# Kernel tuning notes

Measured on AMD Instinct MI355X. Metric: run time of the kernel, lower is better.

The kernel has to match this reference:

```python
import jax, jax.numpy as jnp
import numpy as np

N, E, D, A = 50000, 1_600_000, 32, 2
H1, C1, H2, C2 = 4, 16, 2, 32  # GATv2Conv(D,16,heads=4) -> 64; GATv2Conv(64,32,heads=2) -> 64


def setup_inputs() -> dict:
    key = jax.random.key(0)
    ks = jax.random.split(key, 16)

    def glorot(k, shape):
        fan = shape[0] + shape[-1]
        return jax.random.normal(k, shape, jnp.float32) * np.float32(np.sqrt(2.0 / fan))

    return {
        "x": jax.random.normal(ks[0], (N, D), jnp.float32),
        "edge_index": jax.random.randint(ks[1], (2, E), 0, N),
        "edge_attr": jax.random.normal(ks[2], (E, 2), jnp.float32),
        # GATv2 layer 1 (lin_l/lin_r with bias, lin_edge no bias, att [H,C], out bias)
        "w1_l": glorot(ks[3], (D, H1 * C1)), "b1_l": jnp.zeros((H1 * C1,), jnp.float32),
        "w1_r": glorot(ks[4], (D, H1 * C1)), "b1_r": jnp.zeros((H1 * C1,), jnp.float32),
        "w1_e": glorot(ks[5], (2, H1 * C1)),
        "att1": glorot(ks[6], (H1, C1)),
        "bias1": jnp.zeros((H1 * C1,), jnp.float32),
        # GATv2 layer 2
        "w2_l": glorot(ks[7], (H1 * C1, H2 * C2)), "b2_l": jnp.zeros((H2 * C2,), jnp.float32),
        "w2_r": glorot(ks[8], (H1 * C1, H2 * C2)), "b2_r": jnp.zeros((H2 * C2,), jnp.float32),
        "w2_e": glorot(ks[9], (2, H2 * C2)),
        "att2": glorot(ks[10], (H2, C2)),
        "bias2": jnp.zeros((H2 * C2,), jnp.float32),
        # heads
        "w_actor": glorot(ks[11], (H2 * C2, A)), "b_actor": jnp.zeros((A,), jnp.float32),
        "w_critic": glorot(ks[12], (H2 * C2, 1)), "b_critic": jnp.zeros((1,), jnp.float32),
        "log_std": jnp.zeros((A,), jnp.float32),
    }


def _gatv2(x, src, dst, eattr, Wl, bl, Wr, br, We, att, bias, H, C, n):
    # PyG GATv2Conv: message j->i with i = dst, j = src
    xl = (x @ Wl + bl).reshape(n, H, C)  # source-side transform (x_j)
    xr = (x @ Wr + br).reshape(n, H, C)  # target-side transform (x_i)
    ee = (eattr @ We).reshape(-1, H, C)  # per-edge embedding
    z = jax.nn.leaky_relu(xl[src] + xr[dst] + ee, 0.2)  # [Etot, H, C]
    logits = jnp.einsum('ehc,hc->eh', z, att)  # [Etot, H]
    # segment softmax over incoming edges of each dst node
    m = jax.ops.segment_max(logits, dst, num_segments=n)
    p = jnp.exp(logits - m[dst])
    denom = jax.ops.segment_sum(p, dst, num_segments=n)
    alpha = p / denom[dst]  # every node has a self-loop -> denom > 0
    msg = xl[src] * alpha[:, :, None]  # [Etot, H, C]
    out = jax.ops.segment_sum(msg, dst, num_segments=n)
    return out.reshape(n, H * C) + bias


def reference(x, edge_index, edge_attr,
              w1_l, b1_l, w1_r, b1_r, w1_e, att1, bias1,
              w2_l, b2_l, w2_r, b2_r, w2_e, att2, bias2,
              w_actor, b_actor, w_critic, b_critic, log_std):
    src, dst = edge_index[0], edge_index[1]
    # add_self_loops=True, fill_value='mean': self-loop edge_attr = mean of incoming edge_attr
    cnt = jax.ops.segment_sum(jnp.ones((edge_attr.shape[0],), x.dtype), dst, num_segments=N)
    sums = jax.ops.segment_sum(edge_attr, dst, num_segments=N)
    loop_attr = sums / jnp.maximum(cnt, 1.0)[:, None]
    loop = jnp.arange(N, dtype=src.dtype)
    src_f = jnp.concatenate([src, loop])
    dst_f = jnp.concatenate([dst, loop])
    ea = jnp.concatenate([edge_attr, loop_attr], axis=0)

    h = jax.nn.relu(_gatv2(x, src_f, dst_f, ea, w1_l, b1_l, w1_r, b1_r, w1_e, att1, bias1, H1, C1, N))
    h = jax.nn.relu(_gatv2(h, src_f, dst_f, ea, w2_l, b2_l, w2_r, b2_r, w2_e, att2, bias2, H2, C2, N))

    action_mean = jnp.tanh(h @ w_actor + b_actor)  # [N, A]
    value = h @ w_critic + b_critic               # [N, 1]
    std = jnp.exp(log_std)                        # [A]  (Normal(action_mean, std))
    return action_mean, std, value
```

## Files before the change

kernel.cpp:

```cpp
#include <hip/hip_runtime.h>
#include <hip/hip_fp16.h>
#include <math.h>

#define DIN   32
#define F1    64
#define F2    64

typedef __attribute__((ext_vector_type(2))) float f32x2;

__device__ __forceinline__ f32x2 pkfma(f32x2 a, f32x2 b, f32x2 c) {
#if __has_builtin(__builtin_elementwise_fma)
    return __builtin_elementwise_fma(a, b, c);
#else
    return a * b + c;
#endif
}
__device__ __forceinline__ f32x2 pkmax(f32x2 a, f32x2 b) {
    f32x2 r; r.x = fmaxf(a.x, b.x); r.y = fmaxf(a.y, b.y); return r;
}

__device__ __forceinline__ unsigned bf16pack(float a, float b) {
    unsigned ua = __float_as_uint(a);
    unsigned ub = __float_as_uint(b);
    ua = (ua + 0x7FFFu + ((ua >> 16) & 1u)) >> 16;
    ub = (ub + 0x7FFFu + ((ub >> 16) & 1u)) >> 16;
    return ua | (ub << 16);
}

template <int K>
__device__ __forceinline__ void lin_lr_body(int bid,
        const float* __restrict__ x,
        const float* __restrict__ Wl, const float* __restrict__ bl,
        const float* __restrict__ Wr, const float* __restrict__ br,
        __half* __restrict__ xl, float* __restrict__ xr, int n) {
    __shared__ float Ash[32][K + 4];
    __shared__ float Wsh[K][128];
    const int t = threadIdx.x;
    const int node0 = bid * 32;

    for (int idx = t; idx < 32 * (K / 4); idx += 256) {
        int m = idx / (K / 4), kq = idx % (K / 4);
        float4 v = make_float4(0.f, 0.f, 0.f, 0.f);
        if (node0 + m < n) v = ((const float4*)(x + (size_t)(node0 + m) * K))[kq];
        *(float4*)&Ash[m][kq * 4] = v;
    }
    for (int idx = t; idx < K * 32; idx += 256) {
        int k = idx / 32, j4 = idx % 32;
        float4 v = (j4 < 16) ? ((const float4*)(Wl + (size_t)k * 64))[j4]
                             : ((const float4*)(Wr + (size_t)k * 64))[j4 - 16];
        *(float4*)&Wsh[k][j4 * 4] = v;
    }
    __syncthreads();

    const int ty = t >> 4;
    const int tx = t & 15;
    f32x2 c0[4], c1[4];
#pragma unroll
    for (int j = 0; j < 4; j++) {
        c0[j].x = 0.f; c0[j].y = 0.f;
        c1[j].x = 0.f; c1[j].y = 0.f;
    }

#pragma unroll 4
    for (int k = 0; k < K; k++) {
        float a0 = Ash[ty * 2 + 0][k];
        float a1 = Ash[ty * 2 + 1][k];
        float4 w0 = *(const float4*)&Wsh[k][tx * 8];
        float4 w1 = *(const float4*)&Wsh[k][tx * 8 + 4];
        f32x2 wv0; wv0.x = w0.x; wv0.y = w0.y;
        f32x2 wv1; wv1.x = w0.z; wv1.y = w0.w;
        f32x2 wv2; wv2.x = w1.x; wv2.y = w1.y;
        f32x2 wv3; wv3.x = w1.z; wv3.y = w1.w;
        f32x2 a0s; a0s.x = a0; a0s.y = a0;
        f32x2 a1s; a1s.x = a1; a1s.y = a1;
        c0[0] = pkfma(a0s, wv0, c0[0]);
        c0[1] = pkfma(a0s, wv1, c0[1]);
        c0[2] = pkfma(a0s, wv2, c0[2]);
        c0[3] = pkfma(a0s, wv3, c0[3]);
        c1[0] = pkfma(a1s, wv0, c1[0]);
        c1[1] = pkfma(a1s, wv1, c1[1]);
        c1[2] = pkfma(a1s, wv2, c1[2]);
        c1[3] = pkfma(a1s, wv3, c1[3]);
    }

    const float* bsrc = (tx < 8) ? bl : br;
    int jb = (tx < 8) ? tx * 8 : (tx - 8) * 8;
    float4 b0 = ((const float4*)(bsrc + jb))[0];
    float4 b1 = ((const float4*)(bsrc + jb))[1];
#pragma unroll
    for (int m = 0; m < 2; m++) {
        int node = node0 + ty * 2 + m;
        if (node >= n) continue;
        const f32x2* cc = (m == 0) ? c0 : c1;
        float o0 = cc[0].x + b0.x, o1 = cc[0].y + b0.y;
        float o2 = cc[1].x + b0.z, o3 = cc[1].y + b0.w;
        float o4 = cc[2].x + b1.x, o5 = cc[2].y + b1.y;
        float o6 = cc[3].x + b1.z, o7 = cc[3].y + b1.w;
        if (tx < 8) {
            __half2 h0 = __floats2half2_rn(o0, o1);
            __half2 h1 = __floats2half2_rn(o2, o3);
            __half2 h2 = __floats2half2_rn(o4, o5);
            __half2 h3 = __floats2half2_rn(o6, o7);
            uint4 pk;
            pk.x = *(unsigned*)&h0; pk.y = *(unsigned*)&h1;
            pk.z = *(unsigned*)&h2; pk.w = *(unsigned*)&h3;
            *((uint4*)(xl + (size_t)node * 64 + jb)) = pk;
        } else {
            float4 f0 = make_float4(o0, o1, o2, o3);
            float4 f1 = make_float4(o4, o5, o6, o7);
            ((float4*)(xr + (size_t)node * 64 + jb))[0] = f0;
            ((float4*)(xr + (size_t)node * 64 + jb))[1] = f1;
        }
    }
}

__global__ __launch_bounds__(256, 2)
void fused_bcount_lin1(const int* __restrict__ dstr, int* __restrict__ cursor,
                       int* __restrict__ chunkoff, int* __restrict__ rank,
                       int E, int Ec, int NB, int gridLin,
                       const float* __restrict__ x,
                       const float* __restrict__ Wl, const float* __restrict__ bl,
                       const float* __restrict__ Wr, const float* __restrict__ br,
                       __half* __restrict__ xl, float* __restrict__ xr, int n) {
    __shared__ int hist[256];
    if ((int)blockIdx.x < gridLin) {
        lin_lr_body<DIN>(blockIdx.x, x, Wl, bl, Wr, br, xl, xr, n);
        return;
    }
    const int blk = blockIdx.x - gridLin;
    const int t = threadIdx.x;
    hist[t] = 0;
    __syncthreads();
    const int s0 = blk * Ec, s1 = min(E, s0 + Ec);
    for (int e = s0 + t; e < s1; e += 256)
        rank[e] = atomicAdd(&hist[dstr[e] >> 8], 1);
    __syncthreads();
    if (t < NB) {
        int h = hist[t];
        chunkoff[blk * 256 + t] = h ? atomicAdd(&cursor[t], h) : 0;
    }
}

__global__ __launch_bounds__(512)
void scatter_buckets(const int* __restrict__ srcr, const int* __restrict__ dstr,
                     const float* __restrict__ ea, const int* __restrict__ rank,
                     const int* __restrict__ chunkoff,
                     int2* __restrict__ inter, int E, int Ec, int NB, int cap) {
    __shared__ int colsh[256];
    const int blk = blockIdx.x;
    const int t = threadIdx.x;
    if (t < 256) colsh[t] = (t < NB) ? (t * cap + chunkoff[blk * 256 + t]) : 0;
    __syncthreads();
    const int s0 = blk * Ec, s1 = min(E, s0 + Ec);
    for (int e = s0 + t; e < s1; e += 512) {
        int d = dstr[e];
        float2 v = ((const float2*)ea)[e];
        int2 r;
        r.x = srcr[e] | ((d & 255) << 24);
        r.y = (int)bf16pack(v.x, v.y);
        inter[colsh[d >> 8] + rank[e]] = r;
    }
}

__global__ __launch_bounds__(512)
void bucket_csr(const int2* __restrict__ inter, const int* __restrict__ cursor,
                int2* __restrict__ rse, float2* __restrict__ la2,
                int2* __restrict__ edges, int NB, int N, int cap) {
    __shared__ int sh[256];
    __shared__ int cur[256];
    const int b = blockIdx.x, t = threadIdx.x;
    const int bstart = b * cap;
    const int bend = bstart + cursor[b];

    if (t < 256) sh[t] = 0;
    __syncthreads();
    for (int pos = bstart + t; pos < bend; pos += 512)
        atomicAdd(&sh[((unsigned)inter[pos].x) >> 24], 1);
    __syncthreads();
    int cnt_v = 0, myrs = 0;
    if (t < 256) cnt_v = sh[t];
    __syncthreads();
    if (t < 256) sh[t] = cnt_v;
    __syncthreads();
    for (int off = 1; off < 256; off <<= 1) {
        int x = (t >= off && t < 256) ? sh[t - off] : 0;
        __syncthreads();
        if (t < 256) sh[t] += x;
        __syncthreads();
    }
    if (t < 256) {
        int excl = sh[t] - cnt_v;
        cur[t] = excl;
        myrs = bstart + excl;
        int node = b * 256 + t;
        if (node < N) rse[node] = make_int2(myrs, myrs + cnt_v);
    }
    __syncthreads();
    for (int pos = bstart + t; pos < bend; pos += 512) {
        int2 r = inter[pos];
        int k = atomicAdd(&cur[((unsigned)r.x) >> 24], 1);
        r.x &= 0x00FFFFFF;
        edges[bstart + k] = r;
    }
    int zend = (b + 1) * cap + ((b == NB - 1) ? 64 : 0);
    for (int pos = bend + t; pos < zend; pos += 512)
        edges[pos] = make_int2(0, 0);
    __syncthreads();
    if (t < 256) {
        int node = b * 256 + t;
        if (node < N) {
            float s0 = 0.f, s1 = 0.f;
            for (int pos = myrs; pos < myrs + cnt_v; pos++) {
                int2 rec = edges[pos];
                s0 += __int_as_float(rec.y << 16);
                s1 += __int_as_float(rec.y & 0xFFFF0000);
            }
            float inv = cnt_v ? 1.0f / (float)cnt_v : 0.f;
            la2[node] = make_float2(s0 * inv, s1 * inv);
        }
    }
}

__global__ __launch_bounds__(256, 2)
void lin_lr_tiled64(const float* __restrict__ x,
                    const float* __restrict__ Wl, const float* __restrict__ bl,
                    const float* __restrict__ Wr, const float* __restrict__ br,
                    __half* __restrict__ xl, float* __restrict__ xr, int n) {
    lin_lr_body<F1>(blockIdx.x, x, Wl, bl, Wr, br, xl, xr, n);
}

template <int H, int C, bool FUSE_HEADS>
__global__ __launch_bounds__(256)
void gat_kernel(const __half* __restrict__ xl, const float* __restrict__ xr,
                const int2* __restrict__ rse, const float2* __restrict__ la2,
                const int2* __restrict__ edges,
                const float* __restrict__ We, const float* __restrict__ att,
                const float* __restrict__ bias, float* __restrict__ hout,
                const float* __restrict__ wa, const float* __restrict__ ba,
                const float* __restrict__ wc, const float* __restrict__ bc,
                const float* __restrict__ ls, float* __restrict__ pout,
                int n) {
    constexpr int LPH = C / 4;
    if (FUSE_HEADS && blockIdx.x == 0 && threadIdx.x < 2)
        pout[(size_t)n * 2 + threadIdx.x] = expf(ls[threadIdx.x]);
    const int lane = threadIdx.x & 63;
    const int wid = (blockIdx.x * blockDim.x + threadIdx.x) >> 6;
    if (wid >= n) return;
    const int i = wid;
    const int g = lane >> 4;
    const int q = lane & 15;

    const uint2* xlh = (const uint2*)xl;
    const float4 xri4 = ((const float4*)(xr + (size_t)i * 64))[q];
    const float4 we04 = ((const float4*)We)[q];
    const float4 we14 = ((const float4*)(We + 64))[q];
    const float4 av4 = ((const float4*)att)[q];
    const float LOG2E = 1.4426950408889634f;
    f32x2 xrlo; xrlo.x = xri4.x; xrlo.y = xri4.y;
    f32x2 xrhi; xrhi.x = xri4.z; xrhi.y = xri4.w;
    f32x2 we0lo; we0lo.x = we04.x; we0lo.y = we04.y;
    f32x2 we0hi; we0hi.x = we04.z; we0hi.y = we04.w;
    f32x2 we1lo; we1lo.x = we14.x; we1lo.y = we14.y;
    f32x2 we1hi; we1hi.x = we14.z; we1hi.y = we14.w;
    f32x2 avlo; avlo.x = av4.x * LOG2E; avlo.y = av4.y * LOG2E;
    f32x2 avhi; avhi.x = av4.z * LOG2E; avhi.y = av4.w * LOG2E;

    auto h4lo = [](uint2 h) -> f32x2 {
        float2 a = __half22float2(*(__half2*)&h.x);
        f32x2 r; r.x = a.x; r.y = a.y; return r;
    };
    auto h4hi = [](uint2 h) -> f32x2 {
        float2 b = __half22float2(*(__half2*)&h.y);
        f32x2 r; r.x = b.x; r.y = b.y; return r;
    };
    auto logit_of = [&](f32x2 xlo, f32x2 xhi, float ea0, float ea1) -> float {
        f32x2 e0; e0.x = ea0; e0.y = ea0;
        f32x2 e1; e1.x = ea1; e1.y = ea1;
        f32x2 ylo = xlo + pkfma(e0, we0lo, pkfma(e1, we1lo, xrlo));
        f32x2 yhi = xhi + pkfma(e0, we0hi, pkfma(e1, we1hi, xrhi));
        ylo = pkmax(ylo, ylo * 0.2f);
        yhi = pkmax(yhi, yhi * 0.2f);
        f32x2 l2 = pkfma(ylo, avlo, yhi * avhi);
        return l2.x + l2.y;
    };

    float den = 0.f;
    f32x2 aclo; aclo.x = 0.f; aclo.y = 0.f;
    f32x2 achi; achi.x = 0.f; achi.y = 0.f;

    const int2 se = rse[i];
    const int e0 = se.x, e1 = se.y;
    const int r = (e1 - e0) & 7;

    if (r) {
        int2 h0 = edges[e0 + g];
        int2 h1 = edges[e0 + 4 + g];
        uint2 u0 = xlh[(h0.x << 4) + q];
        uint2 u1 = xlh[(h1.x << 4) + q];
        f32x2 x0lo = h4lo(u0), x0hi = h4hi(u0);
        f32x2 x1lo = h4lo(u1), x1hi = h4hi(u1);
        const bool v0 = g < r;
        const bool v1 = (4 + g) < r;
        float ea00 = v0 ? __int_as_float(h0.y << 16) : 0.f;
        float ea01 = v0 ? __int_as_float(h0.y & 0xFFFF0000) : 0.f;
        float ea10 = v1 ? __int_as_float(h1.y << 16) : 0.f;
        float ea11 = v1 ? __int_as_float(h1.y & 0xFFFF0000) : 0.f;
        float l0 = logit_of(x0lo, x0hi, ea00, ea01);
        float l1 = logit_of(x1lo, x1hi, ea10, ea11);
#pragma unroll
        for (int m = 1; m < LPH; m <<= 1) {
            l0 += __shfl_xor(l0, m, 64);
            l1 += __shfl_xor(l1, m, 64);
        }
        float p0 = v0 ? exp2f(l0) : 0.f;
        float p1 = v1 ? exp2f(l1) : 0.f;
        den += p0 + p1;
        f32x2 p0s; p0s.x = p0; p0s.y = p0;
        f32x2 p1s; p1s.x = p1; p1s.y = p1;
        aclo = pkfma(p0s, x0lo, pkfma(p1s, x1lo, aclo));
        achi = pkfma(p0s, x0hi, pkfma(p1s, x1hi, achi));
    }

    const int em = e0 + r;
    int2 rn0 = edges[em + g];
    int2 rn1 = edges[em + 4 + g];
    uint2 xpn0 = xlh[(rn0.x << 4) + q];
    uint2 xpn1 = xlh[(rn1.x << 4) + q];

    for (int eb = em; eb < e1; eb += 8) {
        int2 r0 = rn0, r1 = rn1;
        f32x2 x0lo = h4lo(xpn0), x0hi = h4hi(xpn0);
        f32x2 x1lo = h4lo(xpn1), x1hi = h4hi(xpn1);
        rn0 = edges[eb + 8 + g];
        rn1 = edges[eb + 12 + g];
        xpn0 = xlh[(rn0.x << 4) + q];
        xpn1 = xlh[(rn1.x << 4) + q];

        float ea00 = __int_as_float(r0.y << 16);
        float ea01 = __int_as_float(r0.y & 0xFFFF0000);
        float ea10 = __int_as_float(r1.y << 16);
        float ea11 = __int_as_float(r1.y & 0xFFFF0000);

        float l0 = logit_of(x0lo, x0hi, ea00, ea01);
        float l1 = logit_of(x1lo, x1hi, ea10, ea11);
#pragma unroll
        for (int m = 1; m < LPH; m <<= 1) {
            l0 += __shfl_xor(l0, m, 64);
            l1 += __shfl_xor(l1, m, 64);
        }
        float p0 = exp2f(l0);
        float p1 = exp2f(l1);
        den += p0 + p1;
        f32x2 p0s; p0s.x = p0; p0s.y = p0;
        f32x2 p1s; p1s.x = p1; p1s.y = p1;
        aclo = pkfma(p0s, x0lo, pkfma(p1s, x1lo, aclo));
        achi = pkfma(p0s, x0hi, pkfma(p1s, x1hi, achi));
    }

    float a0 = aclo.x, a1 = aclo.y, a2 = achi.x, a3 = achi.y;

#pragma unroll
    for (int m = 16; m < 64; m <<= 1) {
        den += __shfl_xor(den, m, 64);
        a0 += __shfl_xor(a0, m, 64);
        a1 += __shfl_xor(a1, m, 64);
        a2 += __shfl_xor(a2, m, 64);
        a3 += __shfl_xor(a3, m, 64);
    }

    const float2 lam = la2[i];
    uint2 us = xlh[(i << 4) + q];
    f32x2 xslo = h4lo(us), xshi = h4hi(us);
    {
        float l = logit_of(xslo, xshi, lam.x, lam.y);
#pragma unroll
        for (int m = 1; m < LPH; m <<= 1) l += __shfl_xor(l, m, 64);
        float p = exp2f(l);
        den += p;
        a0 = fmaf(p, xslo.x, a0);
        a1 = fmaf(p, xslo.y, a1);
        a2 = fmaf(p, xshi.x, a2);
        a3 = fmaf(p, xshi.y, a3);
    }

    float rd = 1.0f / den;
    const float4 bv = ((const float4*)bias)[q];
    float4 o;
    o.x = fmaxf(fmaf(a0, rd, bv.x), 0.f);
    o.y = fmaxf(fmaf(a1, rd, bv.y), 0.f);
    o.z = fmaxf(fmaf(a2, rd, bv.z), 0.f);
    o.w = fmaxf(fmaf(a3, rd, bv.w), 0.f);

    if (!FUSE_HEADS) {
        if (g == 0) ((float4*)(hout + (size_t)i * 64))[q] = o;
    } else {
        float4 wa01 = ((const float4*)wa)[q * 2];
        float4 wa23 = ((const float4*)wa)[q * 2 + 1];
        float4 wcv  = ((const float4*)wc)[q];
        float d0 = o.x * wa01.x + o.y * wa01.z + o.z * wa23.x + o.w * wa23.z;
        float d1 = o.x * wa01.y + o.y * wa01.w + o.z * wa23.y + o.w * wa23.w;
        float d2 = o.x * wcv.x + o.y * wcv.y + o.z * wcv.z + o.w * wcv.w;
#pragma unroll
        for (int m = 1; m < 16; m <<= 1) {
            d0 += __shfl_xor(d0, m, 64);
            d1 += __shfl_xor(d1, m, 64);
            d2 += __shfl_xor(d2, m, 64);
        }
        if (lane == 0) {
            pout[(size_t)i * 2 + 0] = tanhf(d0 + ba[0]);
            pout[(size_t)i * 2 + 1] = tanhf(d1 + ba[1]);
            pout[(size_t)n * 2 + 2 + i] = d2 + bc[0];
        }
    }
}


extern "C" void kernel_launch(void* const* d_in, const int* in_sizes, int n_in,
                              void* d_out, int out_size, void* d_ws, size_t ws_size,
                              hipStream_t stream) {
    const float* x    = (const float*)d_in[0];
    const int*   ei   = (const int*)  d_in[1];
    const float* ea   = (const float*)d_in[2];
    const float* w1l  = (const float*)d_in[3];
    const float* b1l  = (const float*)d_in[4];
    const float* w1r  = (const float*)d_in[5];
    const float* b1r  = (const float*)d_in[6];
    const float* w1e  = (const float*)d_in[7];
    const float* att1 = (const float*)d_in[8];
    const float* bias1= (const float*)d_in[9];
    const float* w2l  = (const float*)d_in[10];
    const float* b2l  = (const float*)d_in[11];
    const float* w2r  = (const float*)d_in[12];
    const float* b2r  = (const float*)d_in[13];
    const float* w2e  = (const float*)d_in[14];
    const float* att2 = (const float*)d_in[15];
    const float* bias2= (const float*)d_in[16];
    const float* wa   = (const float*)d_in[17];
    const float* ba   = (const float*)d_in[18];
    const float* wc   = (const float*)d_in[19];
    const float* bc   = (const float*)d_in[20];
    const float* ls   = (const float*)d_in[21];

    const int N = in_sizes[0] / DIN;
    const int E = in_sizes[2] / 2;
    const int* srcr = ei;
    const int* dstr = ei + E;

    const int NB = (N + 255) >> 8;
    const int Ec = (E + 255) / 256;
    int cap = (E + NB - 1) / NB;
    cap = ((cap + cap / 4) + 63) & ~63;

    char* p = (char*)d_ws;
    auto alloc = [&](size_t bytes) -> void* {
        void* r = (void*)p;
        p += (bytes + 255) & ~(size_t)255;
        return r;
    };
    int*    cursor   = (int*)   alloc(256 * 4);
    int*    chunkoff = (int*)   alloc(256 * 256 * 4);
    int*    rank     = (int*)   alloc((size_t)E * 4);
    int2*   rse      = (int2*)  alloc((size_t)N * 8);
    float2* la2      = (float2*)alloc((size_t)N * 8);
    int2*   edges    = (int2*)  alloc(((size_t)NB * cap + 64) * 8);
    __half* xl       = (__half*)alloc((size_t)N * F1 * 2);
    float*  xr       = (float*) alloc((size_t)N * F1 * 4);
    float*  h1       = (float*) alloc((size_t)N * F1 * 4);
    float*  h2       = (float*) alloc((size_t)N * F2 * 4);
    int2* inter = (int2*)h1;
    (void)ws_size; (void)n_in; (void)out_size;

    hipMemsetAsync(cursor, 0, 256 * 4, stream);

    const int TB = 256;
    int gridGemm = (N + 31) / 32;
    int gridWave = (N + 3) / 4;

    fused_bcount_lin1<<<gridGemm + 256, TB, 0, stream>>>(
        dstr, cursor, chunkoff, rank, E, Ec, NB, gridGemm,
        x, w1l, b1l, w1r, b1r, xl, xr, N);
    scatter_buckets<<<256, 512, 0, stream>>>(srcr, dstr, ea, rank, chunkoff,
                                             inter, E, Ec, NB, cap);
    bucket_csr<<<NB, 512, 0, stream>>>(inter, cursor, rse, la2, edges, NB, N, cap);

    gat_kernel<4, 16, false><<<gridWave, TB, 0, stream>>>(
        xl, xr, rse, la2, edges, w1e, att1, bias1, h1,
        nullptr, nullptr, nullptr, nullptr, nullptr, nullptr, N);
    lin_lr_tiled64<<<gridGemm, TB, 0, stream>>>(h1, w2l, b2l, w2r, b2r, xl, xr, N);
    gat_kernel<2, 32, true><<<gridWave, TB, 0, stream>>>(
        xl, xr, rse, la2, edges, w2e, att2, bias2, h2,
        wa, ba, wc, bc, ls, (float*)d_out, N);
}
```

Before: 297.6 us.

## Split GAT aggregation into two feature-half passes with separate head kernel

Each GAT layer now runs as two launches, each covering 32 of the 64 features. Every wave processes 16 edges per iteration with 8 lanes per edge instead of 4 lanes over 8 edges. The gathered source-feature working set per pass is halved, which is meant to improve cache hit rates on the random xl gathers. In exchange, the edge list is read twice and the per-edge logit work is redone. The actor/critic heads move out of the second GAT kernel into their own kernel that reads h2, adding a launch and an extra pass over h2.

```diff
diff --git a/kernel.cpp b/kernel.cpp
--- a/kernel.cpp
+++ b/kernel.cpp
@@ -229,32 +229,27 @@
     lin_lr_body<F1>(blockIdx.x, x, Wl, bl, Wr, br, xl, xr, n);
 }
 
-template <int H, int C, bool FUSE_HEADS>
+template <int LPH>
 __global__ __launch_bounds__(256)
-void gat_kernel(const __half* __restrict__ xl, const float* __restrict__ xr,
-                const int2* __restrict__ rse, const float2* __restrict__ la2,
-                const int2* __restrict__ edges,
-                const float* __restrict__ We, const float* __restrict__ att,
-                const float* __restrict__ bias, float* __restrict__ hout,
-                const float* __restrict__ wa, const float* __restrict__ ba,
-                const float* __restrict__ wc, const float* __restrict__ bc,
-                const float* __restrict__ ls, float* __restrict__ pout,
-                int n) {
-    constexpr int LPH = C / 4;
-    if (FUSE_HEADS && blockIdx.x == 0 && threadIdx.x < 2)
-        pout[(size_t)n * 2 + threadIdx.x] = expf(ls[threadIdx.x]);
+void gat_slice(const __half* __restrict__ xl, const float* __restrict__ xr,
+               const int2* __restrict__ rse, const float2* __restrict__ la2,
+               const int2* __restrict__ edges,
+               const float* __restrict__ We, const float* __restrict__ att,
+               const float* __restrict__ bias, float* __restrict__ hout,
+               int n, int slice) {
     const int lane = threadIdx.x & 63;
     const int wid = (blockIdx.x * blockDim.x + threadIdx.x) >> 6;
     if (wid >= n) return;
     const int i = wid;
-    const int g = lane >> 4;
-    const int q = lane & 15;
+    const int g = lane >> 3;
+    const int q = lane & 7;
+    const int so2 = slice * 8;
 
     const uint2* xlh = (const uint2*)xl;
-    const float4 xri4 = ((const float4*)(xr + (size_t)i * 64))[q];
-    const float4 we04 = ((const float4*)We)[q];
-    const float4 we14 = ((const float4*)(We + 64))[q];
-    const float4 av4 = ((const float4*)att)[q];
+    const float4 xri4 = ((const float4*)(xr + (size_t)i * 64 + slice * 32))[q];
+    const float4 we04 = ((const float4*)(We + slice * 32))[q];
+    const float4 we14 = ((const float4*)(We + 64 + slice * 32))[q];
+    const float4 av4  = ((const float4*)(att + slice * 32))[q];
     const float LOG2E = 1.4426950408889634f;
     f32x2 xrlo; xrlo.x = xri4.x; xrlo.y = xri4.y;
     f32x2 xrhi; xrhi.x = xri4.z; xrhi.y = xri4.w;
@@ -290,17 +285,17 @@
 
     const int2 se = rse[i];
     const int e0 = se.x, e1 = se.y;
-    const int r = (e1 - e0) & 7;
+    const int r = (e1 - e0) & 15;
 
     if (r) {
         int2 h0 = edges[e0 + g];
-        int2 h1 = edges[e0 + 4 + g];
-        uint2 u0 = xlh[(h0.x << 4) + q];
-        uint2 u1 = xlh[(h1.x << 4) + q];
+        int2 h1 = edges[e0 + 8 + g];
+        uint2 u0 = xlh[(h0.x << 4) + so2 + q];
+        uint2 u1 = xlh[(h1.x << 4) + so2 + q];
         f32x2 x0lo = h4lo(u0), x0hi = h4hi(u0);
         f32x2 x1lo = h4lo(u1), x1hi = h4hi(u1);
         const bool v0 = g < r;
-        const bool v1 = (4 + g) < r;
+        const bool v1 = (8 + g) < r;
         float ea00 = v0 ? __int_as_float(h0.y << 16) : 0.f;
         float ea01 = v0 ? __int_as_float(h0.y & 0xFFFF0000) : 0.f;
         float ea10 = v1 ? __int_as_float(h1.y << 16) : 0.f;
@@ -323,18 +318,18 @@
 
     const int em = e0 + r;
     int2 rn0 = edges[em + g];
-    int2 rn1 = edges[em + 4 + g];
-    uint2 xpn0 = xlh[(rn0.x << 4) + q];
-    uint2 xpn1 = xlh[(rn1.x << 4) + q];
-
-    for (int eb = em; eb < e1; eb += 8) {
+    int2 rn1 = edges[em + 8 + g];
+    uint2 xpn0 = xlh[(rn0.x << 4) + so2 + q];
+    uint2 xpn1 = xlh[(rn1.x << 4) + so2 + q];
+
+    for (int eb = em; eb < e1; eb += 16) {
         int2 r0 = rn0, r1 = rn1;
         f32x2 x0lo = h4lo(xpn0), x0hi = h4hi(xpn0);
         f32x2 x1lo = h4lo(xpn1), x1hi = h4hi(xpn1);
-        rn0 = edges[eb + 8 + g];
-        rn1 = edges[eb + 12 + g];
-        xpn0 = xlh[(rn0.x << 4) + q];
-        xpn1 = xlh[(rn1.x << 4) + q];
+        rn0 = edges[eb + 16 + g];
+        rn1 = edges[eb + 24 + g];
+        xpn0 = xlh[(rn0.x << 4) + so2 + q];
+        xpn1 = xlh[(rn1.x << 4) + so2 + q];
 
         float ea00 = __int_as_float(r0.y << 16);
         float ea01 = __int_as_float(r0.y & 0xFFFF0000);
@@ -360,7 +355,7 @@
     float a0 = aclo.x, a1 = aclo.y, a2 = achi.x, a3 = achi.y;
 
 #pragma unroll
-    for (int m = 16; m < 64; m <<= 1) {
+    for (int m = 8; m < 64; m <<= 1) {
         den += __shfl_xor(den, m, 64);
         a0 += __shfl_xor(a0, m, 64);
         a1 += __shfl_xor(a1, m, 64);
@@ -369,7 +364,7 @@
     }
 
     const float2 lam = la2[i];
-    uint2 us = xlh[(i << 4) + q];
+    uint2 us = xlh[(i << 4) + so2 + q];
     f32x2 xslo = h4lo(us), xshi = h4hi(us);
     {
         float l = logit_of(xslo, xshi, lam.x, lam.y);
@@ -384,33 +379,49 @@
     }
 
     float rd = 1.0f / den;
-    const float4 bv = ((const float4*)bias)[q];
+    const float4 bv = ((const float4*)(bias + slice * 32))[q];
     float4 o;
     o.x = fmaxf(fmaf(a0, rd, bv.x), 0.f);
     o.y = fmaxf(fmaf(a1, rd, bv.y), 0.f);
     o.z = fmaxf(fmaf(a2, rd, bv.z), 0.f);
     o.w = fmaxf(fmaf(a3, rd, bv.w), 0.f);
 
-    if (!FUSE_HEADS) {
-        if (g == 0) ((float4*)(hout + (size_t)i * 64))[q] = o;
-    } else {
-        float4 wa01 = ((const float4*)wa)[q * 2];
-        float4 wa23 = ((const float4*)wa)[q * 2 + 1];
-        float4 wcv  = ((const float4*)wc)[q];
-        float d0 = o.x * wa01.x + o.y * wa01.z + o.z * wa23.x + o.w * wa23.z;
-        float d1 = o.x * wa01.y + o.y * wa01.w + o.z * wa23.y + o.w * wa23.w;
-        float d2 = o.x * wcv.x + o.y * wcv.y + o.z * wcv.z + o.w * wcv.w;
-#pragma unroll
-        for (int m = 1; m < 16; m <<= 1) {
-            d0 += __shfl_xor(d0, m, 64);
-            d1 += __shfl_xor(d1, m, 64);
-            d2 += __shfl_xor(d2, m, 64);
-        }
-        if (lane == 0) {
-            pout[(size_t)i * 2 + 0] = tanhf(d0 + ba[0]);
-            pout[(size_t)i * 2 + 1] = tanhf(d1 + ba[1]);
-            pout[(size_t)n * 2 + 2 + i] = d2 + bc[0];
-        }
+    if (g == 0)
+        ((float4*)(hout + (size_t)i * 64 + slice * 32))[q] = o;
+}
+
+__global__ __launch_bounds__(256)
+void actor_critic_head(const float* __restrict__ h2,
+                       const float* __restrict__ wa, const float* __restrict__ ba,
+                       const float* __restrict__ wc, const float* __restrict__ bc,
+                       const float* __restrict__ ls, float* __restrict__ pout,
+                       int n) {
+    if (blockIdx.x == 0 && threadIdx.x < 2)
+        pout[(size_t)n * 2 + threadIdx.x] = expf(ls[threadIdx.x]);
+    const int lane = threadIdx.x & 63;
+    const int sub = lane >> 4;
+    const int q = lane & 15;
+    const int wid = (blockIdx.x * blockDim.x + threadIdx.x) >> 6;
+    const int i = wid * 4 + sub;
+    if (i >= n) return;
+
+    float4 o = ((const float4*)(h2 + (size_t)i * 64))[q];
+    float4 wa01 = ((const float4*)wa)[q * 2];
+    float4 wa23 = ((const float4*)wa)[q * 2 + 1];
+    float4 wcv  = ((const float4*)wc)[q];
+    float d0 = o.x * wa01.x + o.y * wa01.z + o.z * wa23.x + o.w * wa23.z;
+    float d1 = o.x * wa01.y + o.y * wa01.w + o.z * wa23.y + o.w * wa23.w;
+    float d2 = o.x * wcv.x + o.y * wcv.y + o.z * wcv.z + o.w * wcv.w;
+#pragma unroll
+    for (int m = 1; m < 16; m <<= 1) {
+        d0 += __shfl_xor(d0, m, 64);
+        d1 += __shfl_xor(d1, m, 64);
+        d2 += __shfl_xor(d2, m, 64);
+    }
+    if (q == 0) {
+        pout[(size_t)i * 2 + 0] = tanhf(d0 + ba[0]);
+        pout[(size_t)i * 2 + 1] = tanhf(d1 + ba[1]);
+        pout[(size_t)n * 2 + 2 + i] = d2 + bc[0];
     }
 }
 
@@ -475,6 +486,7 @@
     const int TB = 256;
     int gridGemm = (N + 31) / 32;
     int gridWave = (N + 3) / 4;
+    int gridHead = (N + 15) / 16;
 
     fused_bcount_lin1<<<gridGemm + 256, TB, 0, stream>>>(
         dstr, cursor, chunkoff, rank, E, Ec, NB, gridGemm,
@@ -483,11 +495,18 @@
                                              inter, E, Ec, NB, cap);
     bucket_csr<<<NB, 512, 0, stream>>>(inter, cursor, rse, la2, edges, NB, N, cap);
 
-    gat_kernel<4, 16, false><<<gridWave, TB, 0, stream>>>(
-        xl, xr, rse, la2, edges, w1e, att1, bias1, h1,
-        nullptr, nullptr, nullptr, nullptr, nullptr, nullptr, N);
+    gat_slice<4><<<gridWave, TB, 0, stream>>>(
+        xl, xr, rse, la2, edges, w1e, att1, bias1, h1, N, 0);
+    gat_slice<4><<<gridWave, TB, 0, stream>>>(
+        xl, xr, rse, la2, edges, w1e, att1, bias1, h1, N, 1);
+
     lin_lr_tiled64<<<gridGemm, TB, 0, stream>>>(h1, w2l, b2l, w2r, b2r, xl, xr, N);
-    gat_kernel<2, 32, true><<<gridWave, TB, 0, stream>>>(
-        xl, xr, rse, la2, edges, w2e, att2, bias2, h2,
-        wa, ba, wc, bc, ls, (float*)d_out, N);
-}
+
+    gat_slice<8><<<gridWave, TB, 0, stream>>>(
+        xl, xr, rse, la2, edges, w2e, att2, bias2, h2, N, 0);
+    gat_slice<8><<<gridWave, TB, 0, stream>>>(
+        xl, xr, rse, la2, edges, w2e, att2, bias2, h2, N, 1);
+
+    actor_critic_head<<<gridHead, TB, 0, stream>>>(
+        h2, wa, ba, wc, bc, ls, (float*)d_out, N);
+}
```

Result: slower. 347.8 us (+16.9%).

## Replace two-level bucket CSR build with global per-node atomic count, scan, scatter

Applied to the files above, without the earlier changes.

The two-level bucketed CSR construction (per-chunk bucket histogram, scatter into padded buckets, per-bucket local sort) is replaced by per-node global atomic counting, a block-level prefix scan that recomputes the running prefix sum in each block, and a direct scatter into the final edge array. The self-loop mean edge attribute is no longer precomputed per node. Instead the GAT kernel accumulates edge-attribute sums while it walks the incoming edges and divides by the degree, which removes the separate la2 array. The intent is to drop one full pass over the edges and the padded intermediate buffer. The cost is global atomics contended on 50k counters, a scan whose per-block prefix loop re-reads up to N counters, and extra shuffle reductions in both GAT passes.

```diff
diff --git a/kernel.cpp b/kernel.cpp
--- a/kernel.cpp
+++ b/kernel.cpp
@@ -115,109 +115,71 @@
 }
 
 __global__ __launch_bounds__(256, 2)
-void fused_bcount_lin1(const int* __restrict__ dstr, int* __restrict__ cursor,
-                       int* __restrict__ chunkoff, int* __restrict__ rank,
-                       int E, int Ec, int NB, int gridLin,
-                       const float* __restrict__ x,
-                       const float* __restrict__ Wl, const float* __restrict__ bl,
-                       const float* __restrict__ Wr, const float* __restrict__ br,
-                       __half* __restrict__ xl, float* __restrict__ xr, int n) {
-    __shared__ int hist[256];
+void fused_count_lin1(const int* __restrict__ dstr, int* __restrict__ cnt,
+                      int* __restrict__ rank, int E, int Ec, int gridLin,
+                      const float* __restrict__ x,
+                      const float* __restrict__ Wl, const float* __restrict__ bl,
+                      const float* __restrict__ Wr, const float* __restrict__ br,
+                      __half* __restrict__ xl, float* __restrict__ xr, int n) {
     if ((int)blockIdx.x < gridLin) {
         lin_lr_body<DIN>(blockIdx.x, x, Wl, bl, Wr, br, xl, xr, n);
         return;
     }
     const int blk = blockIdx.x - gridLin;
     const int t = threadIdx.x;
-    hist[t] = 0;
-    __syncthreads();
     const int s0 = blk * Ec, s1 = min(E, s0 + Ec);
     for (int e = s0 + t; e < s1; e += 256)
-        rank[e] = atomicAdd(&hist[dstr[e] >> 8], 1);
+        rank[e] = atomicAdd(&cnt[dstr[e]], 1);
+}
+
+__global__ __launch_bounds__(256)
+void scan_rse(const int* __restrict__ cnt, int2* __restrict__ rse,
+              int2* __restrict__ edges, int N, int E) {
+    __shared__ int sh[256];
+    const int b = blockIdx.x, t = threadIdx.x;
+    if (b == 0 && t < 64) edges[E + t] = make_int2(0, 0);
+    const int base = b * 256;
+    int pre = 0;
+    for (int idx = t; idx < base; idx += 256) pre += cnt[idx];
+    sh[t] = pre;
+    for (int off = 128; off > 0; off >>= 1) {
+        __syncthreads();
+        if (t < off) sh[t] += sh[t + off];
+    }
     __syncthreads();
-    if (t < NB) {
-        int h = hist[t];
-        chunkoff[blk * 256 + t] = h ? atomicAdd(&cursor[t], h) : 0;
+    const int off0 = sh[0];
+    __syncthreads();
+    const int node = base + t;
+    const int c = (node < N) ? cnt[node] : 0;
+    sh[t] = c;
+    __syncthreads();
+    for (int off = 1; off < 256; off <<= 1) {
+        int x = (t >= off) ? sh[t - off] : 0;
+        __syncthreads();
+        sh[t] += x;
+        __syncthreads();
+    }
+    if (node < N) {
+        int excl = sh[t] - c;
+        rse[node] = make_int2(off0 + excl, off0 + excl + c);
     }
 }
 
 __global__ __launch_bounds__(512)
-void scatter_buckets(const int* __restrict__ srcr, const int* __restrict__ dstr,
-                     const float* __restrict__ ea, const int* __restrict__ rank,
-                     const int* __restrict__ chunkoff,
-                     int2* __restrict__ inter, int E, int Ec, int NB, int cap) {
-    __shared__ int colsh[256];
+void scatter_edges(const int* __restrict__ srcr, const int* __restrict__ dstr,
+                   const float* __restrict__ ea, const int* __restrict__ rank,
+                   const int2* __restrict__ rse, int2* __restrict__ edges,
+                   int E, int Ec) {
     const int blk = blockIdx.x;
     const int t = threadIdx.x;
-    if (t < 256) colsh[t] = (t < NB) ? (t * cap + chunkoff[blk * 256 + t]) : 0;
-    __syncthreads();
     const int s0 = blk * Ec, s1 = min(E, s0 + Ec);
     for (int e = s0 + t; e < s1; e += 512) {
         int d = dstr[e];
         float2 v = ((const float2*)ea)[e];
         int2 r;
-        r.x = srcr[e] | ((d & 255) << 24);
+        r.x = srcr[e];
         r.y = (int)bf16pack(v.x, v.y);
-        inter[colsh[d >> 8] + rank[e]] = r;
-    }
-}
-
-__global__ __launch_bounds__(512)
-void bucket_csr(const int2* __restrict__ inter, const int* __restrict__ cursor,
-                int2* __restrict__ rse, float2* __restrict__ la2,
-                int2* __restrict__ edges, int NB, int N, int cap) {
-    __shared__ int sh[256];
-    __shared__ int cur[256];
-    const int b = blockIdx.x, t = threadIdx.x;
-    const int bstart = b * cap;
-    const int bend = bstart + cursor[b];
-
-    if (t < 256) sh[t] = 0;
-    __syncthreads();
-    for (int pos = bstart + t; pos < bend; pos += 512)
-        atomicAdd(&sh[((unsigned)inter[pos].x) >> 24], 1);
-    __syncthreads();
-    int cnt_v = 0, myrs = 0;
-    if (t < 256) cnt_v = sh[t];
-    __syncthreads();
-    if (t < 256) sh[t] = cnt_v;
-    __syncthreads();
-    for (int off = 1; off < 256; off <<= 1) {
-        int x = (t >= off && t < 256) ? sh[t - off] : 0;
-        __syncthreads();
-        if (t < 256) sh[t] += x;
-        __syncthreads();
-    }
-    if (t < 256) {
-        int excl = sh[t] - cnt_v;
-        cur[t] = excl;
-        myrs = bstart + excl;
-        int node = b * 256 + t;
-        if (node < N) rse[node] = make_int2(myrs, myrs + cnt_v);
-    }
-    __syncthreads();
-    for (int pos = bstart + t; pos < bend; pos += 512) {
-        int2 r = inter[pos];
-        int k = atomicAdd(&cur[((unsigned)r.x) >> 24], 1);
-        r.x &= 0x00FFFFFF;
-        edges[bstart + k] = r;
-    }
-    int zend = (b + 1) * cap + ((b == NB - 1) ? 64 : 0);
-    for (int pos = bend + t; pos < zend; pos += 512)
-        edges[pos] = make_int2(0, 0);
-    __syncthreads();
-    if (t < 256) {
-        int node = b * 256 + t;
-        if (node < N) {
-            float s0 = 0.f, s1 = 0.f;
-            for (int pos = myrs; pos < myrs + cnt_v; pos++) {
-                int2 rec = edges[pos];
-                s0 += __int_as_float(rec.y << 16);
-                s1 += __int_as_float(rec.y & 0xFFFF0000);
-            }
-            float inv = cnt_v ? 1.0f / (float)cnt_v : 0.f;
-            la2[node] = make_float2(s0 * inv, s1 * inv);
-        }
+        edges[rse[d].x + rank[e]] = r;
     }
 }
 
@@ -232,7 +194,7 @@
 template <int H, int C, bool FUSE_HEADS>
 __global__ __launch_bounds__(256)
 void gat_kernel(const __half* __restrict__ xl, const float* __restrict__ xr,
-                const int2* __restrict__ rse, const float2* __restrict__ la2,
+                const int2* __restrict__ rse,
                 const int2* __restrict__ edges,
                 const float* __restrict__ We, const float* __restrict__ att,
                 const float* __restrict__ bias, float* __restrict__ hout,
@@ -285,6 +247,7 @@
     };
 
     float den = 0.f;
+    float sea0 = 0.f, sea1 = 0.f;
     f32x2 aclo; aclo.x = 0.f; aclo.y = 0.f;
     f32x2 achi; achi.x = 0.f; achi.y = 0.f;
 
@@ -305,6 +268,8 @@
         float ea01 = v0 ? __int_as_float(h0.y & 0xFFFF0000) : 0.f;
         float ea10 = v1 ? __int_as_float(h1.y << 16) : 0.f;
         float ea11 = v1 ? __int_as_float(h1.y & 0xFFFF0000) : 0.f;
+        sea0 += ea00 + ea10;
+        sea1 += ea01 + ea11;
         float l0 = logit_of(x0lo, x0hi, ea00, ea01);
         float l1 = logit_of(x1lo, x1hi, ea10, ea11);
 #pragma unroll
@@ -340,6 +305,8 @@
         float ea01 = __int_as_float(r0.y & 0xFFFF0000);
         float ea10 = __int_as_float(r1.y << 16);
         float ea11 = __int_as_float(r1.y & 0xFFFF0000);
+        sea0 += ea00 + ea10;
+        sea1 += ea01 + ea11;
 
         float l0 = logit_of(x0lo, x0hi, ea00, ea01);
         float l1 = logit_of(x1lo, x1hi, ea10, ea11);
@@ -366,13 +333,18 @@
         a1 += __shfl_xor(a1, m, 64);
         a2 += __shfl_xor(a2, m, 64);
         a3 += __shfl_xor(a3, m, 64);
-    }
-
-    const float2 lam = la2[i];
+        sea0 += __shfl_xor(sea0, m, 64);
+        sea1 += __shfl_xor(sea1, m, 64);
+    }
+
+    const int cnt_i = e1 - e0;
+    const float invc = cnt_i ? 1.0f / (float)cnt_i : 0.f;
+    const float lamx = sea0 * invc;
+    const float lamy = sea1 * invc;
     uint2 us = xlh[(i << 4) + q];
     f32x2 xslo = h4lo(us), xshi = h4hi(us);
     {
-        float l = logit_of(xslo, xshi, lam.x, lam.y);
+        float l = logit_of(xslo, xshi, lamx, lamy);
 #pragma unroll
         for (int m = 1; m < LPH; m <<= 1) l += __shfl_xor(l, m, 64);
         float p = exp2f(l);
@@ -448,8 +420,6 @@
 
     const int NB = (N + 255) >> 8;
     const int Ec = (E + 255) / 256;
-    int cap = (E + NB - 1) / NB;
-    cap = ((cap + cap / 4) + 63) & ~63;
 
     char* p = (char*)d_ws;
     auto alloc = [&](size_t bytes) -> void* {
@@ -457,37 +427,34 @@
         p += (bytes + 255) & ~(size_t)255;
         return r;
     };
-    int*    cursor   = (int*)   alloc(256 * 4);
-    int*    chunkoff = (int*)   alloc(256 * 256 * 4);
-    int*    rank     = (int*)   alloc((size_t)E * 4);
-    int2*   rse      = (int2*)  alloc((size_t)N * 8);
-    float2* la2      = (float2*)alloc((size_t)N * 8);
-    int2*   edges    = (int2*)  alloc(((size_t)NB * cap + 64) * 8);
-    __half* xl       = (__half*)alloc((size_t)N * F1 * 2);
-    float*  xr       = (float*) alloc((size_t)N * F1 * 4);
-    float*  h1       = (float*) alloc((size_t)N * F1 * 4);
-    float*  h2       = (float*) alloc((size_t)N * F2 * 4);
-    int2* inter = (int2*)h1;
+    int*    cnt   = (int*)   alloc((size_t)NB * 256 * 4);
+    int*    rank  = (int*)   alloc((size_t)E * 4);
+    int2*   rse   = (int2*)  alloc((size_t)N * 8);
+    int2*   edges = (int2*)  alloc(((size_t)E + 64) * 8);
+    __half* xl    = (__half*)alloc((size_t)N * F1 * 2);
+    float*  xr    = (float*) alloc((size_t)N * F1 * 4);
+    float*  h1    = (float*) alloc((size_t)N * F1 * 4);
+    float*  h2    = (float*) alloc((size_t)N * F2 * 4);
     (void)ws_size; (void)n_in; (void)out_size;
 
-    hipMemsetAsync(cursor, 0, 256 * 4, stream);
+    hipMemsetAsync(cnt, 0, (size_t)NB * 256 * 4, stream);
 
     const int TB = 256;
     int gridGemm = (N + 31) / 32;
     int gridWave = (N + 3) / 4;
 
-    fused_bcount_lin1<<<gridGemm + 256, TB, 0, stream>>>(
-        dstr, cursor, chunkoff, rank, E, Ec, NB, gridGemm,
+    fused_count_lin1<<<gridGemm + 256, TB, 0, stream>>>(
+        dstr, cnt, rank, E, Ec, gridGemm,
         x, w1l, b1l, w1r, b1r, xl, xr, N);
-    scatter_buckets<<<256, 512, 0, stream>>>(srcr, dstr, ea, rank, chunkoff,
-                                             inter, E, Ec, NB, cap);
-    bucket_csr<<<NB, 512, 0, stream>>>(inter, cursor, rse, la2, edges, NB, N, cap);
+    scan_rse<<<NB, 256, 0, stream>>>(cnt, rse, edges, N, E);
+    scatter_edges<<<256, 512, 0, stream>>>(srcr, dstr, ea, rank, rse,
+                                           edges, E, Ec);
 
     gat_kernel<4, 16, false><<<gridWave, TB, 0, stream>>>(
-        xl, xr, rse, la2, edges, w1e, att1, bias1, h1,
+        xl, xr, rse, edges, w1e, att1, bias1, h1,
         nullptr, nullptr, nullptr, nullptr, nullptr, nullptr, N);
     lin_lr_tiled64<<<gridGemm, TB, 0, stream>>>(h1, w2l, b2l, w2r, b2r, xl, xr, N);
     gat_kernel<2, 32, true><<<gridWave, TB, 0, stream>>>(
-        xl, xr, rse, la2, edges, w2e, att2, bias2, h2,
+        xl, xr, rse, edges, w2e, att2, bias2, h2,
         wa, ba, wc, bc, ls, (float*)d_out, N);
 }
```

Result: slower. 360.9 us (+21.3%).

## Fuse bucket count with scatter and compute self-loop edge mean inside GAT kernel

Applied to the files above, without the earlier changes.

The bucket histogram and scatter phases are merged into one kernel. Per-edge ranks are kept in shared memory as 16-bit values instead of going through global rank/chunkoff arrays, and the number of chunks rises to 512 so each chunk fits the shared buffer. The serial per-node self-loop mean loop in bucket_csr is removed. The GAT kernels instead accumulate edge-attribute sums while walking each node's edges and reduce them across the wavefront, which saves a launch and global round trips in exchange for a few extra shuffles per node. Both GAT layers recompute the mean, and the 3584-entry shared buffer assumes the edge count per chunk stays within that bound.

```diff
diff --git a/kernel.cpp b/kernel.cpp
--- a/kernel.cpp
+++ b/kernel.cpp
@@ -115,57 +115,49 @@
 }
 
 __global__ __launch_bounds__(256, 2)
-void fused_bcount_lin1(const int* __restrict__ dstr, int* __restrict__ cursor,
-                       int* __restrict__ chunkoff, int* __restrict__ rank,
-                       int E, int Ec, int NB, int gridLin,
-                       const float* __restrict__ x,
-                       const float* __restrict__ Wl, const float* __restrict__ bl,
-                       const float* __restrict__ Wr, const float* __restrict__ br,
-                       __half* __restrict__ xl, float* __restrict__ xr, int n) {
+void fused_scatter_lin1(const int* __restrict__ srcr, const int* __restrict__ dstr,
+                        const float* __restrict__ ea, int* __restrict__ cursor,
+                        int2* __restrict__ inter,
+                        int E, int Ec, int NB, int cap, int gridCnt,
+                        const float* __restrict__ x,
+                        const float* __restrict__ Wl, const float* __restrict__ bl,
+                        const float* __restrict__ Wr, const float* __restrict__ br,
+                        __half* __restrict__ xl, float* __restrict__ xr, int n) {
+    if ((int)blockIdx.x >= gridCnt) {
+        lin_lr_body<DIN>(blockIdx.x - gridCnt, x, Wl, bl, Wr, br, xl, xr, n);
+        return;
+    }
     __shared__ int hist[256];
-    if ((int)blockIdx.x < gridLin) {
-        lin_lr_body<DIN>(blockIdx.x, x, Wl, bl, Wr, br, xl, xr, n);
-        return;
-    }
-    const int blk = blockIdx.x - gridLin;
+    __shared__ int colsh[256];
+    __shared__ unsigned short rksh[3584];
+    const int blk = blockIdx.x;
     const int t = threadIdx.x;
     hist[t] = 0;
     __syncthreads();
     const int s0 = blk * Ec, s1 = min(E, s0 + Ec);
     for (int e = s0 + t; e < s1; e += 256)
-        rank[e] = atomicAdd(&hist[dstr[e] >> 8], 1);
+        rksh[e - s0] = (unsigned short)atomicAdd(&hist[dstr[e] >> 8], 1);
     __syncthreads();
     if (t < NB) {
         int h = hist[t];
-        chunkoff[blk * 256 + t] = h ? atomicAdd(&cursor[t], h) : 0;
-    }
-}
-
-__global__ __launch_bounds__(512)
-void scatter_buckets(const int* __restrict__ srcr, const int* __restrict__ dstr,
-                     const float* __restrict__ ea, const int* __restrict__ rank,
-                     const int* __restrict__ chunkoff,
-                     int2* __restrict__ inter, int E, int Ec, int NB, int cap) {
-    __shared__ int colsh[256];
-    const int blk = blockIdx.x;
-    const int t = threadIdx.x;
-    if (t < 256) colsh[t] = (t < NB) ? (t * cap + chunkoff[blk * 256 + t]) : 0;
-    __syncthreads();
-    const int s0 = blk * Ec, s1 = min(E, s0 + Ec);
-    for (int e = s0 + t; e < s1; e += 512) {
+        int off = h ? atomicAdd(&cursor[t], h) : 0;
+        colsh[t] = t * cap + off;
+    }
+    __syncthreads();
+    for (int e = s0 + t; e < s1; e += 256) {
         int d = dstr[e];
         float2 v = ((const float2*)ea)[e];
         int2 r;
         r.x = srcr[e] | ((d & 255) << 24);
         r.y = (int)bf16pack(v.x, v.y);
-        inter[colsh[d >> 8] + rank[e]] = r;
+        inter[colsh[d >> 8] + (int)rksh[e - s0]] = r;
     }
 }
 
 __global__ __launch_bounds__(512)
 void bucket_csr(const int2* __restrict__ inter, const int* __restrict__ cursor,
-                int2* __restrict__ rse, float2* __restrict__ la2,
-                int2* __restrict__ edges, int NB, int N, int cap) {
+                int2* __restrict__ rse, int2* __restrict__ edges,
+                int NB, int N, int cap) {
     __shared__ int sh[256];
     __shared__ int cur[256];
     const int b = blockIdx.x, t = threadIdx.x;
@@ -177,7 +169,7 @@
     for (int pos = bstart + t; pos < bend; pos += 512)
         atomicAdd(&sh[((unsigned)inter[pos].x) >> 24], 1);
     __syncthreads();
-    int cnt_v = 0, myrs = 0;
+    int cnt_v = 0;
     if (t < 256) cnt_v = sh[t];
     __syncthreads();
     if (t < 256) sh[t] = cnt_v;
@@ -191,7 +183,7 @@
     if (t < 256) {
         int excl = sh[t] - cnt_v;
         cur[t] = excl;
-        myrs = bstart + excl;
+        int myrs = bstart + excl;
         int node = b * 256 + t;
         if (node < N) rse[node] = make_int2(myrs, myrs + cnt_v);
     }
@@ -205,20 +197,6 @@
     int zend = (b + 1) * cap + ((b == NB - 1) ? 64 : 0);
     for (int pos = bend + t; pos < zend; pos += 512)
         edges[pos] = make_int2(0, 0);
-    __syncthreads();
-    if (t < 256) {
-        int node = b * 256 + t;
-        if (node < N) {
-            float s0 = 0.f, s1 = 0.f;
-            for (int pos = myrs; pos < myrs + cnt_v; pos++) {
-                int2 rec = edges[pos];
-                s0 += __int_as_float(rec.y << 16);
-                s1 += __int_as_float(rec.y & 0xFFFF0000);
-            }
-            float inv = cnt_v ? 1.0f / (float)cnt_v : 0.f;
-            la2[node] = make_float2(s0 * inv, s1 * inv);
-        }
-    }
 }
 
 __global__ __launch_bounds__(256, 2)
@@ -232,7 +210,7 @@
 template <int H, int C, bool FUSE_HEADS>
 __global__ __launch_bounds__(256)
 void gat_kernel(const __half* __restrict__ xl, const float* __restrict__ xr,
-                const int2* __restrict__ rse, const float2* __restrict__ la2,
+                const int2* __restrict__ rse,
                 const int2* __restrict__ edges,
                 const float* __restrict__ We, const float* __restrict__ att,
                 const float* __restrict__ bias, float* __restrict__ hout,
@@ -285,6 +263,7 @@
     };
 
     float den = 0.f;
+    float sea0 = 0.f, sea1 = 0.f;
     f32x2 aclo; aclo.x = 0.f; aclo.y = 0.f;
     f32x2 achi; achi.x = 0.f; achi.y = 0.f;
 
@@ -305,6 +284,8 @@
         float ea01 = v0 ? __int_as_float(h0.y & 0xFFFF0000) : 0.f;
         float ea10 = v1 ? __int_as_float(h1.y << 16) : 0.f;
         float ea11 = v1 ? __int_as_float(h1.y & 0xFFFF0000) : 0.f;
+        sea0 += ea00 + ea10;
+        sea1 += ea01 + ea11;
         float l0 = logit_of(x0lo, x0hi, ea00, ea01);
         float l1 = logit_of(x1lo, x1hi, ea10, ea11);
 #pragma unroll
@@ -340,6 +321,8 @@
         float ea01 = __int_as_float(r0.y & 0xFFFF0000);
         float ea10 = __int_as_float(r1.y << 16);
         float ea11 = __int_as_float(r1.y & 0xFFFF0000);
+        sea0 += ea00 + ea10;
+        sea1 += ea01 + ea11;
 
         float l0 = logit_of(x0lo, x0hi, ea00, ea01);
         float l1 = logit_of(x1lo, x1hi, ea10, ea11);
@@ -366,13 +349,18 @@
         a1 += __shfl_xor(a1, m, 64);
         a2 += __shfl_xor(a2, m, 64);
         a3 += __shfl_xor(a3, m, 64);
-    }
-
-    const float2 lam = la2[i];
+        sea0 += __shfl_xor(sea0, m, 64);
+        sea1 += __shfl_xor(sea1, m, 64);
+    }
+
+    const int cnt_i = e1 - e0;
+    const float invc = cnt_i ? 1.0f / (float)cnt_i : 0.f;
+    const float lamx = sea0 * invc;
+    const float lamy = sea1 * invc;
     uint2 us = xlh[(i << 4) + q];
     f32x2 xslo = h4lo(us), xshi = h4hi(us);
     {
-        float l = logit_of(xslo, xshi, lam.x, lam.y);
+        float l = logit_of(xslo, xshi, lamx, lamy);
 #pragma unroll
         for (int m = 1; m < LPH; m <<= 1) l += __shfl_xor(l, m, 64);
         float p = exp2f(l);
@@ -447,7 +435,8 @@
     const int* dstr = ei + E;
 
     const int NB = (N + 255) >> 8;
-    const int Ec = (E + 255) / 256;
+    const int NCH = 512;
+    const int Ec = (E + NCH - 1) / NCH;
     int cap = (E + NB - 1) / NB;
     cap = ((cap + cap / 4) + 63) & ~63;
 
@@ -457,16 +446,13 @@
         p += (bytes + 255) & ~(size_t)255;
         return r;
     };
-    int*    cursor   = (int*)   alloc(256 * 4);
-    int*    chunkoff = (int*)   alloc(256 * 256 * 4);
-    int*    rank     = (int*)   alloc((size_t)E * 4);
-    int2*   rse      = (int2*)  alloc((size_t)N * 8);
-    float2* la2      = (float2*)alloc((size_t)N * 8);
-    int2*   edges    = (int2*)  alloc(((size_t)NB * cap + 64) * 8);
-    __half* xl       = (__half*)alloc((size_t)N * F1 * 2);
-    float*  xr       = (float*) alloc((size_t)N * F1 * 4);
-    float*  h1       = (float*) alloc((size_t)N * F1 * 4);
-    float*  h2       = (float*) alloc((size_t)N * F2 * 4);
+    int*    cursor = (int*)   alloc(256 * 4);
+    int2*   rse    = (int2*)  alloc((size_t)N * 8);
+    int2*   edges  = (int2*)  alloc(((size_t)NB * cap + 64) * 8);
+    __half* xl     = (__half*)alloc((size_t)N * F1 * 2);
+    float*  xr     = (float*) alloc((size_t)N * F1 * 4);
+    float*  h1     = (float*) alloc((size_t)N * F1 * 4);
+    float*  h2     = (float*) alloc((size_t)N * F2 * 4);
     int2* inter = (int2*)h1;
     (void)ws_size; (void)n_in; (void)out_size;
 
@@ -476,18 +462,16 @@
     int gridGemm = (N + 31) / 32;
     int gridWave = (N + 3) / 4;
 
-    fused_bcount_lin1<<<gridGemm + 256, TB, 0, stream>>>(
-        dstr, cursor, chunkoff, rank, E, Ec, NB, gridGemm,
+    fused_scatter_lin1<<<NCH + gridGemm, TB, 0, stream>>>(
+        srcr, dstr, ea, cursor, inter, E, Ec, NB, cap, NCH,
         x, w1l, b1l, w1r, b1r, xl, xr, N);
-    scatter_buckets<<<256, 512, 0, stream>>>(srcr, dstr, ea, rank, chunkoff,
-                                             inter, E, Ec, NB, cap);
-    bucket_csr<<<NB, 512, 0, stream>>>(inter, cursor, rse, la2, edges, NB, N, cap);
+    bucket_csr<<<NB, 512, 0, stream>>>(inter, cursor, rse, edges, NB, N, cap);
 
     gat_kernel<4, 16, false><<<gridWave, TB, 0, stream>>>(
-        xl, xr, rse, la2, edges, w1e, att1, bias1, h1,
+        xl, xr, rse, edges, w1e, att1, bias1, h1,
         nullptr, nullptr, nullptr, nullptr, nullptr, nullptr, N);
     lin_lr_tiled64<<<gridGemm, TB, 0, stream>>>(h1, w2l, b2l, w2r, b2r, xl, xr, N);
     gat_kernel<2, 32, true><<<gridWave, TB, 0, stream>>>(
-        xl, xr, rse, la2, edges, w2e, att2, bias2, h2,
+        xl, xr, rse, edges, w2e, att2, bias2, h2,
         wa, ba, wc, bc, ls, (float*)d_out, N);
 }
```

Result: no change. 294.5 us (-1.0%).
